# Kernel optimization log

Hardware: AMD Instinct MI355X
Metric: run time of the kernel (lower is better)

Reference implementation:

```python
import jax, jax.numpy as jnp
import numpy as np
from jax import lax

K = 8192
D = 256
BETA = 0.1
DECAY = 0.99
EPS = 1e-05


def setup_inputs() -> dict:
    key = jax.random.key(0)
    k1, k2, k3 = jax.random.split(key, 3)
    z_e = jax.random.normal(k1, (8, 2048, D), dtype=jnp.float32)
    codebook = jax.random.normal(k2, (K, D), dtype=jnp.float32)
    ema_cluster_size = jnp.zeros((K,), dtype=jnp.float32)
    ema_w = jax.random.normal(k3, (K, D), dtype=jnp.float32)
    return {"z_e": z_e, "codebook": codebook,
            "ema_cluster_size": ema_cluster_size, "ema_w": ema_w}


def reference(z_e, codebook, ema_cluster_size, ema_w):
    B, L, Dd = z_e.shape
    # squared-distance matrix (B, L, K): ||z||^2 - 2 z.C^T + ||c||^2
    dist = ((z_e ** 2).sum(-1, keepdims=True)
            - 2.0 * jnp.einsum('bld,kd->blk', z_e, codebook)
            + (codebook ** 2).sum(-1))
    codes = jnp.argmin(dist, axis=-1)          # (B, L) int
    z_q = codebook[codes]                      # gather (B, L, D)

    # training-mode EMA statistics (segment_sum == one_hot.T @ z_e, memory-light)
    flat_codes = codes.reshape(-1)
    flat_z = z_e.reshape(-1, Dd)
    n_i = jax.ops.segment_sum(jnp.ones(flat_codes.shape, dtype=z_e.dtype),
                              flat_codes, num_segments=K)
    dw = jax.ops.segment_sum(flat_z, flat_codes, num_segments=K)
    new_cluster_size = DECAY * ema_cluster_size + (1.0 - DECAY) * n_i
    new_ema_w = DECAY * ema_w + (1.0 - DECAY) * dw
    new_codebook = new_ema_w / (new_cluster_size + EPS)[:, None]

    # straight-through combine and commitment loss
    z_q_st = z_e + lax.stop_gradient(z_q - z_e)
    vq_loss = BETA * jnp.mean((z_e - lax.stop_gradient(z_q)) ** 2)
    return z_q_st, codes, vq_loss, new_codebook, new_cluster_size, new_ema_w
```

## Files before the change

kernel.cpp:

```cpp
#include <hip/hip_runtime.h>
#include <hip/hip_bf16.h>
#include <math.h>

#define N_ROWS 16384
#define DIM    256
#define KCODES 8192

#define OFF_ZQ    0
#define OFF_CODES 4194304
#define OFF_LOSS  4210688
#define OFF_CB    4210689
#define OFF_CS    6307841
#define OFF_EW    6316033
#define OUT_TOTAL 8413185

typedef __attribute__((ext_vector_type(8))) short bf16x8;
typedef __attribute__((ext_vector_type(4))) float f32x4;
typedef __attribute__((ext_vector_type(16))) float f32x16;

__device__ __forceinline__ void gll16(const void* g, void* l) {
  __builtin_amdgcn_global_load_lds(
      (const __attribute__((address_space(1))) unsigned int*)g,
      (__attribute__((address_space(3))) unsigned int*)l, 16, 0, 0);
}

__device__ __forceinline__ unsigned short f2bf(float x) {
  __hip_bfloat16 h = __float2bfloat16(x);
  return *reinterpret_cast<unsigned short*>(&h);
}

__device__ __forceinline__ unsigned umin32(unsigned a, unsigned b) { return a < b ? a : b; }
__device__ __forceinline__ unsigned umax32(unsigned a, unsigned b) { return a > b ? a : b; }

__global__ __launch_bounds__(256) void k_cvt(const float* __restrict__ src,
                                             unsigned short* __restrict__ dst,
                                             int n8, int* __restrict__ cnt,
                                             float* __restrict__ loss_part) {
  int i = blockIdx.x * 256 + threadIdx.x;
  if (i < n8) {
    const float4 a = ((const float4*)src)[i * 2];
    const float4 b = ((const float4*)src)[i * 2 + 1];
    union { unsigned short u[8]; uint4 v; } o;
    o.u[0] = f2bf(a.x); o.u[1] = f2bf(a.y); o.u[2] = f2bf(a.z); o.u[3] = f2bf(a.w);
    o.u[4] = f2bf(b.x); o.u[5] = f2bf(b.y); o.u[6] = f2bf(b.z); o.u[7] = f2bf(b.w);
    ((uint4*)dst)[i] = o.v;
  } else if (cnt) {
    int zi = i - n8;
    if (zi < 8192) cnt[zi] = 0;
    else if (zi < 8448) loss_part[zi - 8192] = 0.0f;
  }
}

__global__ __launch_bounds__(256) void k_prep(const float* __restrict__ cb,
                                              unsigned short* __restrict__ cbt,
                                              float* __restrict__ cnormb) {
  const int tid = threadIdx.x;
  const int code = blockIdx.x * 8 + (tid >> 5);
  const int dq = tid & 31;
  const float4 v0 = *(const float4*)(cb + (size_t)code * 256 + dq * 8);
  const float4 v1 = *(const float4*)(cb + (size_t)code * 256 + dq * 8 + 4);
  union { unsigned short u[8]; uint4 q; } o;
  o.u[0] = f2bf(-2.f * v0.x); o.u[1] = f2bf(-2.f * v0.y);
  o.u[2] = f2bf(-2.f * v0.z); o.u[3] = f2bf(-2.f * v0.w);
  o.u[4] = f2bf(-2.f * v1.x); o.u[5] = f2bf(-2.f * v1.y);
  o.u[6] = f2bf(-2.f * v1.z); o.u[7] = f2bf(-2.f * v1.w);
  *(uint4*)(cbt + ((size_t)dq * 8192 + code) * 8) = o.q;
  float s = v0.x * v0.x + v0.y * v0.y + v0.z * v0.z + v0.w * v0.w +
            v1.x * v1.x + v1.y * v1.y + v1.z * v1.z + v1.w * v1.w;
#pragma unroll
  for (int off = 16; off >= 1; off >>= 1) s += __shfl_down(s, off);
  if ((tid & 31) == 0) cnormb[code] = s + 1024.0f;
}

__global__ __launch_bounds__(256, 2) void k_argmin(
    const unsigned short* __restrict__ zb,
    const unsigned short* __restrict__ cbt,
    const float* __restrict__ cnb,
    unsigned long long* __restrict__ partials) {
  __shared__ __align__(16) unsigned char lds[20480];

  const int tid = threadIdx.x;
  const int lane = tid & 63;
  const int w = tid >> 6;
  const int wc = w & 1;
  const int wr = w >> 1;
  const int hi = lane >> 5;
  const int l31 = lane & 31;
  const int chunk = blockIdx.x;
  const int r0 = blockIdx.y << 7;

  gll16((const char*)cnb + (size_t)chunk * 4096 + tid * 16,
        lds + 16384 + tid * 16);
  const char* zgb = (const char*)zb + (size_t)r0 * 512;
#pragma unroll
  for (int it = 0; it < 4; ++it) {
    int s = it * 256 + tid;
    int row = s >> 5;
    int dql = (s & 31) ^ row;
    gll16(zgb + row * 512 + dql * 16, lds + s * 16);
  }

  bf16x8 zr0[16], zr1[16];
#pragma unroll
  for (int p = 0; p < 4; ++p) {
    asm volatile("s_waitcnt vmcnt(0)" ::: "memory");
    __builtin_amdgcn_s_barrier();
    __builtin_amdgcn_sched_barrier(0);
    if ((p >> 1) == wr) {
      const int xr = l31 * 16;
      const int rb = l31 * 512;
      const int hx = hi * 16;
      if ((p & 1) == 0) {
#pragma unroll
        for (int ks = 0; ks < 16; ++ks)
          zr0[ks] = *(const bf16x8*)(lds + rb + ((ks * 32 + hx) ^ xr));
      } else {
#pragma unroll
        for (int ks = 0; ks < 16; ++ks)
          zr1[ks] = *(const bf16x8*)(lds + rb + ((ks * 32 + hx) ^ xr));
      }
    }
    asm volatile("s_waitcnt lgkmcnt(0)" ::: "memory");
    __builtin_amdgcn_sched_barrier(0);
    __builtin_amdgcn_s_barrier();
    if (p < 3) {
#pragma unroll
      for (int it = 0; it < 4; ++it) {
        int s = it * 256 + tid;
        int row = s >> 5;
        int dql = (s & 31) ^ row;
        gll16(zgb + ((p + 1) * 32 + row) * 512 + dql * 16, lds + s * 16);
      }
    }
  }

  const char* cgc = (const char*)cbt + (size_t)hi * 131072 +
                    ((size_t)chunk * 1024 + wc * 64 + l31) * 16;
  bf16x8 p0[4], p1[4];
#pragma unroll
  for (int s = 0; s < 4; ++s) {
    const char* ap = cgc + s * 262144;
    p0[s] = *(const bf16x8*)ap;
    p1[s] = *(const bf16x8*)(ap + 512);
  }

  const unsigned wchi4 = (unsigned)(wc * 64 + hi * 4);
  unsigned k1_00 = 0xFFFFFFFFu, k2_00 = 0xFFFFFFFFu;
  unsigned k1_01 = 0xFFFFFFFFu, k2_01 = 0xFFFFFFFFu;
  unsigned k1_10 = 0xFFFFFFFFu, k2_10 = 0xFFFFFFFFu;
  unsigned k1_11 = 0xFFFFFFFFu, k2_11 = 0xFFFFFFFFu;
  f32x16 acc00, acc01, acc10, acc11;

#define KSTEP(ks, TAIL)                                                        \
  {                                                                            \
    bf16x8 a0 = p0[(ks) & 3], a1 = p1[(ks) & 3];                               \
    if (!(TAIL) || (ks) < 12) {                 \
      const char* ap = cgc + (((ks) + 4) & 15) * 262144 +                      \
                       ((((ks) + 4) >> 4) * 2048);                             \
      p0[(ks) & 3] = *(const bf16x8*)ap;                                       \
      p1[(ks) & 3] = *(const bf16x8*)(ap + 512);                               \
    }                                                                          \
    __builtin_amdgcn_s_setprio(1);                                             \
    acc00 = __builtin_amdgcn_mfma_f32_32x32x16_bf16(a0, zr0[ks], acc00, 0, 0, 0); \
    acc01 = __builtin_amdgcn_mfma_f32_32x32x16_bf16(a0, zr1[ks], acc01, 0, 0, 0); \
    acc10 = __builtin_amdgcn_mfma_f32_32x32x16_bf16(a1, zr0[ks], acc10, 0, 0, 0); \
    acc11 = __builtin_amdgcn_mfma_f32_32x32x16_bf16(a1, zr1[ks], acc11, 0, 0, 0); \
    __builtin_amdgcn_s_setprio(0);                                             \
  }

#define CTBODY(TAIL)                                                           \
  {                                                                            \
    const int cnoff = 16384 + ct * 512 + wc * 256 + hi * 16;                   \
    f32x4 cnA[4], cnB[4];                                                      \
    _Pragma("unroll") for (int g2 = 0; g2 < 4; ++g2) {                         \
      cnA[g2] = *(const f32x4*)(lds + cnoff + g2 * 32);                        \
      cnB[g2] = *(const f32x4*)(lds + cnoff + 128 + g2 * 32);                  \
    }                                                                          \
    _Pragma("unroll") for (int r = 0; r < 16; ++r) {                           \
      float vA = cnA[r >> 2][r & 3], vB = cnB[r >> 2][r & 3];                  \
      acc00[r] = vA; acc01[r] = vA; acc10[r] = vB; acc11[r] = vB;              \
    }                                                                          \
    KSTEP(0, TAIL)  KSTEP(1, TAIL)  KSTEP(2, TAIL)  KSTEP(3, TAIL)             \
    KSTEP(4, TAIL)  KSTEP(5, TAIL)  KSTEP(6, TAIL)  KSTEP(7, TAIL)             \
    KSTEP(8, TAIL)  KSTEP(9, TAIL)  KSTEP(10, TAIL) KSTEP(11, TAIL)            \
    KSTEP(12, TAIL) KSTEP(13, TAIL) KSTEP(14, TAIL) KSTEP(15, TAIL)            \
    const unsigned vb = (unsigned)(ct * 128) | wchi4;                          \
    _Pragma("unroll") for (int r = 0; r < 16; ++r) {                           \
      const unsigned ic = (unsigned)(8 * (r >> 2) + (r & 3));                  \
      unsigned key;                                                            \
      key = (__float_as_uint(acc00[r]) & 0xFFFFFC00u) | vb | ic;               \
      if (key < k1_00) { k2_00 = k1_00; k1_00 = key; } else if (key < k2_00) k2_00 = key; \
      key = (__float_as_uint(acc01[r]) & 0xFFFFFC00u) | vb | ic;               \
      if (key < k1_01) { k2_01 = k1_01; k1_01 = key; } else if (key < k2_01) k2_01 = key; \
      key = (__float_as_uint(acc10[r]) & 0xFFFFFC00u) | vb | ic | 32u;         \
      if (key < k1_10) { k2_10 = k1_10; k1_10 = key; } else if (key < k2_10) k2_10 = key; \
      key = (__float_as_uint(acc11[r]) & 0xFFFFFC00u) | vb | ic | 32u;         \
      if (key < k1_11) { k2_11 = k1_11; k1_11 = key; } else if (key < k2_11) k2_11 = key; \
    }                                                                          \
    cgc += 2048;                                                               \
  }

  for (int ct = 0; ct < 7; ++ct) CTBODY(false)
  { int ct = 7; CTBODY(true) }
#undef CTBODY
#undef KSTEP

#define FIN(K1V, K2V, ZF, CF)                                                  \
  {                                                                            \
    unsigned o1 = (unsigned)__shfl_xor((int)(K1V), 32);                        \
    unsigned o2 = (unsigned)__shfl_xor((int)(K2V), 32);                        \
    unsigned n1 = umin32((K1V), o1);                                           \
    unsigned n2 = umin32(umax32((K1V), o1), umin32((K2V), o2));                \
    if (lane < 32) {                                                           \
      int row = r0 + wr * 64 + (ZF) * 32 + l31;                                \
      partials[(size_t)row * 32 + (chunk * 4 + wc * 2 + (CF))] =               \
          ((unsigned long long)n2 << 32) | n1;                                 \
    }                                                                          \
  }
  FIN(k1_00, k2_00, 0, 0) FIN(k1_10, k2_10, 0, 1)
  FIN(k1_01, k2_01, 1, 0) FIN(k1_11, k2_11, 1, 1)
#undef FIN
}

__global__ __launch_bounds__(256) void k_reduce(
    const unsigned long long* __restrict__ partials, const float* __restrict__ z,
    const float* __restrict__ cb, float* __restrict__ out_codes,
    int* __restrict__ cnt) {
  const int row = blockIdx.x * 4 + (threadIdx.x >> 6);
  const int lane = threadIdx.x & 63;
  const int e = lane & 31;

  unsigned myK1 = 0xFFFFFFFFu, myK2 = 0xFFFFFFFFu;
  if (lane < 32) {
    unsigned long long v = partials[(size_t)row * 32 + e];
    myK1 = (unsigned)v; myK2 = (unsigned)(v >> 32);
  }
  unsigned K1 = myK1, K2 = myK2;
  int bc = e >> 2;
#pragma unroll
  for (int m = 1; m <= 32; m <<= 1) {
    unsigned o1 = (unsigned)__shfl_xor((int)K1, m);
    unsigned o2 = (unsigned)__shfl_xor((int)K2, m);
    int ob = __shfl_xor(bc, m);
    unsigned nK2 = umin32(umax32(K1, o1), umin32(K2, o2));
    if (o1 < K1 || (o1 == K1 && ob < bc)) { K1 = o1; bc = ob; }
    K2 = nK2;
  }
  int chosen = bc * 1024 + (int)(K1 & 1023u);

  float r1 = __uint_as_float(K1 & 0xFFFFFC00u);
  float r2 = __uint_as_float(K2 & 0xFFFFFC00u);
  if (r2 - r1 < 0.75f) {
    const float win = r1 + 0.75f;
    const float* zr = z + ((size_t)row << 8);
    double bestd = 1e300; int bestj = 0x7fffffff;
#pragma unroll
    for (int h = 0; h < 2; ++h) {
      unsigned k = h ? myK2 : myK1;
      float bv = __uint_as_float(k & 0xFFFFFC00u);
      if (lane < 32 && bv <= win) {
        int jv = (e >> 2) * 1024 + (int)(k & 1023u);
        const float* c = cb + ((size_t)jv << 8);
        double d = 0.0;
        for (int kk = 0; kk < DIM; ++kk) {
          double df = (double)zr[kk] - (double)c[kk];
          d += df * df;
        }
        if (d < bestd || (d == bestd && jv < bestj)) { bestd = d; bestj = jv; }
      }
    }
#pragma unroll
    for (int m = 1; m <= 32; m <<= 1) {
      double od = __shfl_xor(bestd, m);
      int oj = __shfl_xor(bestj, m);
      if (od < bestd || (od == bestd && oj < bestj)) { bestd = od; bestj = oj; }
    }
    chosen = bestj;
  }
  if (lane == 0) {
    out_codes[row] = (float)chosen;
    if (cnt) atomicAdd(&cnt[chosen], 1);
  }
}

__global__ __launch_bounds__(1024) void k_scan(
    const int* __restrict__ cnt, int* __restrict__ start,
    int* __restrict__ cursor, const float* __restrict__ ema_cs,
    float* __restrict__ cs_out) {
  const int t = threadIdx.x;
  const int lane = t & 63, wid = t >> 6;
  const int base = t * 8;
  int c[8], s = 0;
#pragma unroll
  for (int i = 0; i < 8; ++i) { c[i] = cnt[base + i]; s += c[i]; }
  int inc = s;
#pragma unroll
  for (int off = 1; off < 64; off <<= 1) {
    int v = __shfl_up(inc, off);
    if (lane >= off) inc += v;
  }
  __shared__ int wsum[16], wbase[16];
  if (lane == 63) wsum[wid] = inc;
  __syncthreads();
  if (t < 16) {
    int v = wsum[t];
    int winc = v;
#pragma unroll
    for (int off = 1; off < 16; off <<= 1) {
      int u = __shfl_up(winc, off);
      if (t >= off) winc += u;
    }
    wbase[t] = winc - v;
  }
  __syncthreads();
  int ex = wbase[wid] + (inc - s);
#pragma unroll
  for (int i = 0; i < 8; ++i) {
    start[base + i] = ex;
    cursor[base + i] = ex;
    cs_out[base + i] = 0.99f * ema_cs[base + i] + 0.01f * (float)c[i];
    ex += c[i];
  }
}

__global__ __launch_bounds__(256) void k_place(const float* __restrict__ codesf,
                                               int* __restrict__ cursor,
                                               int* __restrict__ rowlist) {
  int i = blockIdx.x * 256 + threadIdx.x;
  int c = (int)codesf[i];
  int p = atomicAdd(&cursor[c], 1);
  rowlist[p] = i;
}

__global__ __launch_bounds__(256) void k_dw2(
    const float* __restrict__ z, const float* __restrict__ cb,
    const int* __restrict__ start, const int* __restrict__ cnt,
    const int* __restrict__ rowlist, const float* __restrict__ ema_w,
    const float* __restrict__ cs_new, float* __restrict__ zq,
    float* __restrict__ ew, float* __restrict__ cb_out,
    float* __restrict__ loss_part) {
  const int k = blockIdx.x;
  const int d = threadIdx.x;
  const int s = start[k], n = cnt[k];
  const size_t o = ((size_t)k << 8) + d;
  const float q = cb[o];
  float a0 = 0.f, a1 = 0.f, a2 = 0.f, a3 = 0.f;
  float l0 = 0.f, l1 = 0.f, l2 = 0.f, l3 = 0.f;
  int t = 0;
  for (; t + 4 <= n; t += 4) {
    size_t ro0 = ((size_t)rowlist[s + t] << 8) + d;
    size_t ro1 = ((size_t)rowlist[s + t + 1] << 8) + d;
    size_t ro2 = ((size_t)rowlist[s + t + 2] << 8) + d;
    size_t ro3 = ((size_t)rowlist[s + t + 3] << 8) + d;
    float z0 = z[ro0], z1 = z[ro1], z2 = z[ro2], z3 = z[ro3];
    zq[ro0] = q; zq[ro1] = q; zq[ro2] = q; zq[ro3] = q;
    a0 += z0; a1 += z1; a2 += z2; a3 += z3;
    float d0 = z0 - q, d1 = z1 - q, d2 = z2 - q, d3 = z3 - q;
    l0 += d0 * d0; l1 += d1 * d1; l2 += d2 * d2; l3 += d3 * d3;
  }
  for (; t < n; ++t) {
    size_t ro = ((size_t)rowlist[s + t] << 8) + d;
    float zv = z[ro];
    zq[ro] = q;
    a0 += zv;
    float df = zv - q;
    l0 += df * df;
  }
  float a = (a0 + a1) + (a2 + a3);
  float lacc = (l0 + l1) + (l2 + l3);
  const float v = 0.99f * ema_w[o] + 0.01f * a;
  ew[o] = v;
  cb_out[o] = v / (cs_new[k] + 1e-5f);

#pragma unroll
  for (int off = 32; off >= 1; off >>= 1) lacc += __shfl_down(lacc, off);
  __shared__ float wp[4];
  if ((d & 63) == 0) wp[d >> 6] = lacc;
  __syncthreads();
  if (d == 0 && n > 0) {
    float ssum = (wp[0] + wp[1]) + (wp[2] + wp[3]);
    atomicAdd(loss_part + (k & 255), ssum * (float)(0.1 / 4194304.0));
  }
}

__global__ __launch_bounds__(256) void k_loss_final(
    const float* __restrict__ part, float* __restrict__ loss) {
  float s = part[threadIdx.x];
#pragma unroll
  for (int off = 32; off >= 1; off >>= 1) s += __shfl_down(s, off);
  __shared__ float w[4];
  if ((threadIdx.x & 63) == 0) w[threadIdx.x >> 6] = s;
  __syncthreads();
  if (threadIdx.x == 0) loss[0] = (w[0] + w[1]) + (w[2] + w[3]);
}

__global__ __launch_bounds__(256) void k_scatter(
    const float* __restrict__ z, const float* __restrict__ cb,
    const float* __restrict__ codesf, float* __restrict__ zq,
    float* __restrict__ loss, float* __restrict__ cs_acc,
    float* __restrict__ ew_acc) {
  const int row = blockIdx.x;
  const int d = threadIdx.x;
  const int c = (int)codesf[row];
  const float zv = z[((size_t)row << 8) + d];
  const float qv = cb[((size_t)c << 8) + d];
  zq[((size_t)row << 8) + d] = zv + (qv - zv);
  float diff = zv - qv;
  float sq = diff * diff;
#pragma unroll
  for (int off = 32; off >= 1; off >>= 1) sq += __shfl_down(sq, off);
  __shared__ float wpart[4];
  if ((d & 63) == 0) wpart[d >> 6] = sq;
  __syncthreads();
  if (d == 0) {
    float s = (wpart[0] + wpart[1]) + (wpart[2] + wpart[3]);
    atomicAdd(loss, s * (float)(0.1 / 4194304.0));
    atomicAdd(cs_acc + c, 1.0f);
  }
  atomicAdd(ew_acc + ((size_t)c << 8) + d, zv);
}

__global__ __launch_bounds__(256) void k_ema_cs(const float* __restrict__ ema_cs,
                                                float* __restrict__ cs_io) {
  const int k = blockIdx.x * 256 + threadIdx.x;
  const float cnt = cs_io[k];
  cs_io[k] = 0.99f * ema_cs[k] + 0.01f * cnt;
}

__global__ __launch_bounds__(256) void k_ema_w(const float* __restrict__ ema_w,
                                               const float* __restrict__ cs_new,
                                               float* __restrict__ ew_io,
                                               float* __restrict__ cb_out) {
  const int i = blockIdx.x * 256 + threadIdx.x;
  const float dw = ew_io[i];
  const float v = 0.99f * ema_w[i] + 0.01f * dw;
  ew_io[i] = v;
  cb_out[i] = v / (cs_new[i >> 8] + 1e-5f);
}

extern "C" void kernel_launch(void* const* d_in, const int* in_sizes, int n_in,
                              void* d_out, int out_size, void* d_ws, size_t ws_size,
                              hipStream_t stream) {
  const float* z      = (const float*)d_in[0];
  const float* cb     = (const float*)d_in[1];
  const float* ema_cs = (const float*)d_in[2];
  const float* ema_w  = (const float*)d_in[3];
  float* out = (float*)d_out;

  float* o_zq    = out + OFF_ZQ;
  float* o_codes = out + OFF_CODES;
  float* o_loss  = out + OFF_LOSS;
  float* o_cb    = out + OFF_CB;
  float* o_cs    = out + OFF_CS;
  float* o_ew    = out + OFF_EW;

  uintptr_t zb_a  = ((uintptr_t)o_cb + 15) & ~(uintptr_t)15;
  uintptr_t cbt_a = ((uintptr_t)o_ew + 15) & ~(uintptr_t)15;
  unsigned short* zbuf = (unsigned short*)zb_a;
  unsigned short* cbt  = (unsigned short*)cbt_a;
  float* cnormb = (float*)(cbt_a + 4194304);
  unsigned long long* partials = (unsigned long long*)o_zq;

  const size_t ws_need = 4 * (8192 * 3 + 16384 + 256);
  const bool sorted = (ws_size >= ws_need);
  int* cnt      = (int*)d_ws;
  int* start    = cnt + 8192;
  int* cursor   = start + 8192;
  int* rowlist  = cursor + 8192;
  float* loss_part = (float*)(rowlist + 16384);

  k_cvt <<<2081, 256, 0, stream>>>(z, zbuf, 524288,
                                   sorted ? cnt : (int*)nullptr, loss_part);
  k_prep<<<1024, 256, 0, stream>>>(cb, cbt, cnormb);

  dim3 g(8, 128);
  k_argmin<<<g, 256, 0, stream>>>(zbuf, cbt, cnormb, partials);
  k_reduce<<<N_ROWS / 4, 256, 0, stream>>>(partials, z, cb, o_codes,
                                           sorted ? cnt : (int*)nullptr);

  if (sorted) {
    k_scan <<<1, 1024, 0, stream>>>(cnt, start, cursor, ema_cs, o_cs);
    k_place<<<64, 256, 0, stream>>>(o_codes, cursor, rowlist);
    k_dw2<<<KCODES, 256, 0, stream>>>(z, cb, start, cnt, rowlist, ema_w,
                                      o_cs, o_zq, o_ew, o_cb, loss_part);
    k_loss_final<<<1, 256, 0, stream>>>(loss_part, o_loss);
  } else {
    (void)hipMemsetAsync(o_loss, 0,
                         (size_t)(OUT_TOTAL - OFF_LOSS) * sizeof(float), stream);
    k_scatter<<<N_ROWS, 256, 0, stream>>>(z, cb, o_codes, o_zq, o_loss, o_cs,
                                          o_ew);
    k_ema_cs<<<KCODES / 256, 256, 0, stream>>>(ema_cs, o_cs);
    k_ema_w <<<KCODES * DIM / 256, 256, 0, stream>>>(ema_w, o_cs, o_ew, o_cb);
  }
}
```

Before: 162.3 us.

## Fuse prep kernels, stagger code-tile order per wave, tree-reduce top-2

Merges the z bf16 conversion and the codebook transpose/norm kernels into one launch, which saves a kernel launch and its gap. In the argmin kernel, the two column waves now walk the code tiles in rotated order, and one of them sleeps briefly at the start, to spread out memory and LDS contention. The serial branchy top-2 update over 16 accumulator values is replaced with a branchless min/max tree reduction. These changes add register pressure and alter the prefetch addressing, which could affect occupancy.

```diff
diff --git a/kernel.cpp b/kernel.cpp
--- a/kernel.cpp
+++ b/kernel.cpp
@@ -32,44 +32,42 @@
 __device__ __forceinline__ unsigned umin32(unsigned a, unsigned b) { return a < b ? a : b; }
 __device__ __forceinline__ unsigned umax32(unsigned a, unsigned b) { return a > b ? a : b; }
 
-__global__ __launch_bounds__(256) void k_cvt(const float* __restrict__ src,
-                                             unsigned short* __restrict__ dst,
-                                             int n8, int* __restrict__ cnt,
-                                             float* __restrict__ loss_part) {
-  int i = blockIdx.x * 256 + threadIdx.x;
-  if (i < n8) {
-    const float4 a = ((const float4*)src)[i * 2];
-    const float4 b = ((const float4*)src)[i * 2 + 1];
+__global__ __launch_bounds__(256) void k_pre(
+    const float* __restrict__ z, unsigned short* __restrict__ zbuf,
+    const float* __restrict__ cb, unsigned short* __restrict__ cbt,
+    float* __restrict__ cnormb, int* __restrict__ cnt,
+    float* __restrict__ loss_part) {
+  const int b = blockIdx.x;
+  const int tid = threadIdx.x;
+  if (b < 2048) {
+    int i = b * 256 + tid;
+    const float4 a = ((const float4*)z)[i * 2];
+    const float4 c = ((const float4*)z)[i * 2 + 1];
     union { unsigned short u[8]; uint4 v; } o;
     o.u[0] = f2bf(a.x); o.u[1] = f2bf(a.y); o.u[2] = f2bf(a.z); o.u[3] = f2bf(a.w);
-    o.u[4] = f2bf(b.x); o.u[5] = f2bf(b.y); o.u[6] = f2bf(b.z); o.u[7] = f2bf(b.w);
-    ((uint4*)dst)[i] = o.v;
+    o.u[4] = f2bf(c.x); o.u[5] = f2bf(c.y); o.u[6] = f2bf(c.z); o.u[7] = f2bf(c.w);
+    ((uint4*)zbuf)[i] = o.v;
+  } else if (b < 3072) {
+    const int code = (b - 2048) * 8 + (tid >> 5);
+    const int dq = tid & 31;
+    const float4 v0 = *(const float4*)(cb + (size_t)code * 256 + dq * 8);
+    const float4 v1 = *(const float4*)(cb + (size_t)code * 256 + dq * 8 + 4);
+    union { unsigned short u[8]; uint4 q; } o;
+    o.u[0] = f2bf(-2.f * v0.x); o.u[1] = f2bf(-2.f * v0.y);
+    o.u[2] = f2bf(-2.f * v0.z); o.u[3] = f2bf(-2.f * v0.w);
+    o.u[4] = f2bf(-2.f * v1.x); o.u[5] = f2bf(-2.f * v1.y);
+    o.u[6] = f2bf(-2.f * v1.z); o.u[7] = f2bf(-2.f * v1.w);
+    *(uint4*)(cbt + ((size_t)dq * 8192 + code) * 8) = o.q;
+    float s = v0.x * v0.x + v0.y * v0.y + v0.z * v0.z + v0.w * v0.w +
+              v1.x * v1.x + v1.y * v1.y + v1.z * v1.z + v1.w * v1.w;
+#pragma unroll
+    for (int off = 16; off >= 1; off >>= 1) s += __shfl_down(s, off);
+    if ((tid & 31) == 0) cnormb[code] = s + 1024.0f;
   } else if (cnt) {
-    int zi = i - n8;
+    int zi = (b - 3072) * 256 + tid;
     if (zi < 8192) cnt[zi] = 0;
     else if (zi < 8448) loss_part[zi - 8192] = 0.0f;
   }
-}
-
-__global__ __launch_bounds__(256) void k_prep(const float* __restrict__ cb,
-                                              unsigned short* __restrict__ cbt,
-                                              float* __restrict__ cnormb) {
-  const int tid = threadIdx.x;
-  const int code = blockIdx.x * 8 + (tid >> 5);
-  const int dq = tid & 31;
-  const float4 v0 = *(const float4*)(cb + (size_t)code * 256 + dq * 8);
-  const float4 v1 = *(const float4*)(cb + (size_t)code * 256 + dq * 8 + 4);
-  union { unsigned short u[8]; uint4 q; } o;
-  o.u[0] = f2bf(-2.f * v0.x); o.u[1] = f2bf(-2.f * v0.y);
-  o.u[2] = f2bf(-2.f * v0.z); o.u[3] = f2bf(-2.f * v0.w);
-  o.u[4] = f2bf(-2.f * v1.x); o.u[5] = f2bf(-2.f * v1.y);
-  o.u[6] = f2bf(-2.f * v1.z); o.u[7] = f2bf(-2.f * v1.w);
-  *(uint4*)(cbt + ((size_t)dq * 8192 + code) * 8) = o.q;
-  float s = v0.x * v0.x + v0.y * v0.y + v0.z * v0.z + v0.w * v0.w +
-            v1.x * v1.x + v1.y * v1.y + v1.z * v1.z + v1.w * v1.w;
-#pragma unroll
-  for (int off = 16; off >= 1; off >>= 1) s += __shfl_down(s, off);
-  if ((tid & 31) == 0) cnormb[code] = s + 1024.0f;
 }
 
 __global__ __launch_bounds__(256, 2) void k_argmin(
@@ -134,17 +132,21 @@
     }
   }
 
+  __builtin_amdgcn_sched_barrier(0);
+  if (wc) __builtin_amdgcn_s_sleep(32);
+  __builtin_amdgcn_sched_barrier(0);
+
+  const int wcp = wc * 4;
   const char* cgc = (const char*)cbt + (size_t)hi * 131072 +
                     ((size_t)chunk * 1024 + wc * 64 + l31) * 16;
   bf16x8 p0[4], p1[4];
 #pragma unroll
   for (int s = 0; s < 4; ++s) {
-    const char* ap = cgc + s * 262144;
+    const char* ap = cgc + wcp * 2048 + s * 262144;
     p0[s] = *(const bf16x8*)ap;
     p1[s] = *(const bf16x8*)(ap + 512);
   }
 
-  const unsigned wchi4 = (unsigned)(wc * 64 + hi * 4);
   unsigned k1_00 = 0xFFFFFFFFu, k2_00 = 0xFFFFFFFFu;
   unsigned k1_01 = 0xFFFFFFFFu, k2_01 = 0xFFFFFFFFu;
   unsigned k1_10 = 0xFFFFFFFFu, k2_10 = 0xFFFFFFFFu;
@@ -154,9 +156,9 @@
 #define KSTEP(ks, TAIL)                                                        \
   {                                                                            \
     bf16x8 a0 = p0[(ks) & 3], a1 = p1[(ks) & 3];                               \
-    if (!(TAIL) || (ks) < 12) {                 \
-      const char* ap = cgc + (((ks) + 4) & 15) * 262144 +                      \
-                       ((((ks) + 4) >> 4) * 2048);                             \
+    if (!(TAIL) || (ks) < 12) {                \
+      const char* ap = ((ks) < 12) ? (cgc + coff + ((ks) + 4) * 262144)        \
+                                   : (cgc + noff + ((ks) - 12) * 262144);      \
       p0[(ks) & 3] = *(const bf16x8*)ap;                                       \
       p1[(ks) & 3] = *(const bf16x8*)(ap + 512);                               \
     }                                                                          \
@@ -168,8 +170,44 @@
     __builtin_amdgcn_s_setprio(0);                                             \
   }
 
-#define CTBODY(TAIL)                                                           \
+#define TOP2(ACCV, EXTRA, K1V, K2V)                                            \
   {                                                                            \
+    unsigned kk[16];                                                           \
+    _Pragma("unroll") for (int r = 0; r < 16; ++r)                             \
+      kk[r] = (__float_as_uint(ACCV[r]) & 0xFFFFFC00u) | vb |                  \
+              (unsigned)(8 * (r >> 2) + (r & 3)) | (EXTRA);                    \
+    unsigned a1[8], a2[8];                                                     \
+    _Pragma("unroll") for (int r = 0; r < 8; ++r) {                            \
+      a1[r] = umin32(kk[2 * r], kk[2 * r + 1]);                                \
+      a2[r] = umax32(kk[2 * r], kk[2 * r + 1]);                                \
+    }                                                                          \
+    _Pragma("unroll") for (int r = 0; r < 4; ++r) {                            \
+      unsigned m = umin32(a1[r], a1[r + 4]);                                   \
+      unsigned M = umax32(a1[r], a1[r + 4]);                                   \
+      a2[r] = umin32(M, umin32(a2[r], a2[r + 4]));                             \
+      a1[r] = m;                                                               \
+    }                                                                          \
+    _Pragma("unroll") for (int r = 0; r < 2; ++r) {                            \
+      unsigned m = umin32(a1[r], a1[r + 2]);                                   \
+      unsigned M = umax32(a1[r], a1[r + 2]);                                   \
+      a2[r] = umin32(M, umin32(a2[r], a2[r + 2]));                             \
+      a1[r] = m;                                                               \
+    }                                                                          \
+    {                                                                          \
+      unsigned m = umin32(a1[0], a1[1]);                                       \
+      unsigned M = umax32(a1[0], a1[1]);                                       \
+      unsigned s2 = umin32(M, umin32(a2[0], a2[1]));                           \
+      unsigned nk2 = umin32(umax32(K1V, m), umin32(K2V, s2));                  \
+      K1V = umin32(K1V, m);                                                    \
+      K2V = nk2;                                                               \
+    }                                                                          \
+  }
+
+#define CTBODY(I, TAIL)                                                        \
+  {                                                                            \
+    const int ct = ((I) + wcp) & 7;                                            \
+    const int coff = ct * 2048;                                                \
+    const int noff = ((((I) + 1) + wcp) & 7) * 2048;                           \
     const int cnoff = 16384 + ct * 512 + wc * 256 + hi * 16;                   \
     f32x4 cnA[4], cnB[4];                                                      \
     _Pragma("unroll") for (int g2 = 0; g2 < 4; ++g2) {                         \
@@ -184,25 +222,17 @@
     KSTEP(4, TAIL)  KSTEP(5, TAIL)  KSTEP(6, TAIL)  KSTEP(7, TAIL)             \
     KSTEP(8, TAIL)  KSTEP(9, TAIL)  KSTEP(10, TAIL) KSTEP(11, TAIL)            \
     KSTEP(12, TAIL) KSTEP(13, TAIL) KSTEP(14, TAIL) KSTEP(15, TAIL)            \
-    const unsigned vb = (unsigned)(ct * 128) | wchi4;                          \
-    _Pragma("unroll") for (int r = 0; r < 16; ++r) {                           \
-      const unsigned ic = (unsigned)(8 * (r >> 2) + (r & 3));                  \
-      unsigned key;                                                            \
-      key = (__float_as_uint(acc00[r]) & 0xFFFFFC00u) | vb | ic;               \
-      if (key < k1_00) { k2_00 = k1_00; k1_00 = key; } else if (key < k2_00) k2_00 = key; \
-      key = (__float_as_uint(acc01[r]) & 0xFFFFFC00u) | vb | ic;               \
-      if (key < k1_01) { k2_01 = k1_01; k1_01 = key; } else if (key < k2_01) k2_01 = key; \
-      key = (__float_as_uint(acc10[r]) & 0xFFFFFC00u) | vb | ic | 32u;         \
-      if (key < k1_10) { k2_10 = k1_10; k1_10 = key; } else if (key < k2_10) k2_10 = key; \
-      key = (__float_as_uint(acc11[r]) & 0xFFFFFC00u) | vb | ic | 32u;         \
-      if (key < k1_11) { k2_11 = k1_11; k1_11 = key; } else if (key < k2_11) k2_11 = key; \
-    }                                                                          \
-    cgc += 2048;                                                               \
-  }
-
-  for (int ct = 0; ct < 7; ++ct) CTBODY(false)
-  { int ct = 7; CTBODY(true) }
+    const unsigned vb = (unsigned)(ct * 128) | (unsigned)(wc * 64 + hi * 4);   \
+    TOP2(acc00, 0u,  k1_00, k2_00)                                             \
+    TOP2(acc01, 0u,  k1_01, k2_01)                                             \
+    TOP2(acc10, 32u, k1_10, k2_10)                                             \
+    TOP2(acc11, 32u, k1_11, k2_11)                                             \
+  }
+
+  for (int i = 0; i < 7; ++i) CTBODY(i, false)
+  CTBODY(7, true)
 #undef CTBODY
+#undef TOP2
 #undef KSTEP
 
 #define FIN(K1V, K2V, ZF, CF)                                                  \
@@ -469,9 +499,8 @@
   int* rowlist  = cursor + 8192;
   float* loss_part = (float*)(rowlist + 16384);
 
-  k_cvt <<<2081, 256, 0, stream>>>(z, zbuf, 524288,
-                                   sorted ? cnt : (int*)nullptr, loss_part);
-  k_prep<<<1024, 256, 0, stream>>>(cb, cbt, cnormb);
+  k_pre<<<3105, 256, 0, stream>>>(z, zbuf, cb, cbt, cnormb,
+                                  sorted ? cnt : (int*)nullptr, loss_part);
 
   dim3 g(8, 128);
   k_argmin<<<g, 256, 0, stream>>>(zbuf, cbt, cnormb, partials);
```

Result: slower. 268.9 us (+65.7%).
